# Kernel tuning notes

Hardware: AMD Instinct MI355X
Metric: run time of the kernel (lower is better)

## Reference

```python
import jax, jax.numpy as jnp
import numpy as np

B = 4096          # number of graphs
NPG = 148         # nodes per graph (fixed by ReadOut(num_nodes=148))
N = B * NPG       # total nodes = 606208
EPG = 592         # edges per graph (~avg degree 4: RNA backbone + base pairs)
E = B * EPG       # total edges = 2424832


def setup_inputs() -> dict:
    key = jax.random.key(0)
    ks = jax.random.split(key, 10)
    x = jax.random.normal(ks[0], (N, 4), jnp.float32)
    # edges confined within each graph via per-graph node offsets
    src = jax.random.randint(ks[1], (E,), 0, NPG, dtype=jnp.int32)
    dst = jax.random.randint(ks[2], (E,), 0, NPG, dtype=jnp.int32)
    offs = jnp.repeat(jnp.arange(B, dtype=jnp.int32) * NPG, EPG)
    edge_index = jnp.stack([src + offs, dst + offs], axis=0)
    batch = jnp.repeat(jnp.arange(B, dtype=jnp.int32), NPG)
    # GCNConv weights (glorot-ish) and biases: 4->16->32->64
    def glorot(k, fi, fo):
        return jax.random.normal(k, (fi, fo), jnp.float32) * np.sqrt(2.0 / (fi + fo)).astype(np.float32)
    W1 = glorot(ks[3], 4, 16); b1 = jnp.zeros((16,), jnp.float32)
    W2 = glorot(ks[4], 16, 32); b2 = jnp.zeros((32,), jnp.float32)
    W3 = glorot(ks[5], 32, 64); b3 = jnp.zeros((64,), jnp.float32)
    return {"x": x, "edge_index": edge_index, "batch": batch,
            "W1": W1, "b1": b1, "W2": W2, "b2": b2, "W3": W3, "b3": b3}


def gcn_conv(x, src, dst, W, b, n):
    """PyG GCNConv: x' = D^{-1/2}(A+I)D^{-1/2} (x W) + b."""
    h = x @ W                                   # [n, out]
    loop = jnp.arange(n, dtype=src.dtype)       # self loops
    s = jnp.concatenate([src, loop])
    d = jnp.concatenate([dst, loop])
    deg = jax.ops.segment_sum(jnp.ones_like(s, h.dtype), d, num_segments=n)
    dis = jnp.where(deg > 0, jax.lax.rsqrt(jnp.maximum(deg, 1e-12)), 0.0)
    norm = dis[s] * dis[d]                      # [n_edges_with_loops]
    msg = h[s] * norm[:, None]                  # gather + normalize
    return jax.ops.segment_sum(msg, d, num_segments=n) + b


def reference(x, edge_index, batch, W1, b1, W2, b2, W3, b3):
    src, dst = edge_index[0], edge_index[1]
    n = x.shape[0]
    # Dropout(p=0.1) is identity at inference time
    h = jax.nn.relu(gcn_conv(x, src, dst, W1, b1, n))
    h = jax.nn.relu(gcn_conv(h, src, dst, W2, b2, n))
    h = jax.nn.relu(gcn_conv(h, src, dst, W3, b3, n))
    # to_dense_batch with max_num_nodes=148: every graph has exactly 148 nodes
    # and `batch` is sorted block-constant, so dense batching == reshape.
    dense = h.reshape(B, NPG, h.shape[-1])      # [B, 148, 64]
    return dense.reshape(B, -1)                 # Flatten -> [B, 9472]
```

## Files before the change

### kernel.cpp

```cpp
#include <hip/hip_runtime.h>

#define NPG 148
#define EPG 592
#define NTHR 256
#define SA   40
#define MT   10

typedef _Float16 h8 __attribute__((ext_vector_type(8)));
typedef _Float16 h4 __attribute__((ext_vector_type(4)));
typedef float    f4 __attribute__((ext_vector_type(4)));


template<int Fi, int Fo, int KC, int NTN, int MAXJ, int NSLOT, int WROW, int BOFF, bool LAST>
__device__ __forceinline__ void layer(int t,
    _Float16* __restrict__ A16, const _Float16* __restrict__ Wt,
    const float* __restrict__ s_b, const int* __restrict__ s_csr,
    const int* __restrict__ s_row, const float* __restrict__ s_dis,
    float* __restrict__ gout)
{
    constexpr int GITEMS = NPG * KC;

    float r[NSLOT][8];
    #pragma unroll
    for (int sl = 0; sl < NSLOT; ++sl) {
        const int item = t + sl * NTHR;
        if (item < GITEMS) {
            const int d  = item / KC;
            const int kc = item % KC;
            const h8 hv = *reinterpret_cast<const h8*>(&A16[d * SA + kc * 8]);
            const float dd = s_dis[d];
            float a[8];
            #pragma unroll
            for (int u = 0; u < 8; ++u) a[u] = dd * (float)hv[u];
            const int e1 = s_row[d + 1];
            for (int e = s_row[d]; e < e1; ++e) {
                const int sidx = s_csr[e];
                const float ds = s_dis[sidx];
                const h8 m = *reinterpret_cast<const h8*>(&A16[sidx * SA + kc * 8]);
                #pragma unroll
                for (int u = 0; u < 8; ++u) a[u] = fmaf((float)m[u], ds, a[u]);
            }
            #pragma unroll
            for (int u = 0; u < 8; ++u) r[sl][u] = a[u] * dd;
        }
    }
    __syncthreads();
    #pragma unroll
    for (int sl = 0; sl < NSLOT; ++sl) {
        const int item = t + sl * NTHR;
        if (item < GITEMS) {
            const int d  = item / KC;
            const int kc = item % KC;
            h8 pv;
            #pragma unroll
            for (int u = 0; u < 8; ++u) pv[u] = (_Float16)r[sl][u];
            *reinterpret_cast<h8*>(&A16[d * SA + kc * 8]) = pv;
        }
    }
    __syncthreads();

    const int w   = t >> 6;
    const int l16 = t & 15;
    const int q   = (t >> 4) & 3;
    h8 af[MAXJ], bf[MAXJ];
    #pragma unroll
    for (int j = 0; j < MAXJ; ++j) {
        const int idx = w + 4 * j;
        if (idx < MT * NTN) {
            const int mt = idx / NTN, nt = idx % NTN;
            af[j] = *reinterpret_cast<const h8*>(&A16[(mt * 16 + l16) * SA + q * 8]);
            bf[j] = *reinterpret_cast<const h8*>(&Wt[(WROW + nt * 16 + l16) * SA + q * 8]);
        }
    }
    __syncthreads();
    #pragma unroll
    for (int j = 0; j < MAXJ; ++j) {
        const int idx = w + 4 * j;
        if (idx < MT * NTN) {
            const int mt = idx / NTN, nt = idx % NTN;
            f4 acc = {0.f, 0.f, 0.f, 0.f};
            acc = __builtin_amdgcn_mfma_f32_16x16x32_f16(af[j], bf[j], acc, 0, 0, 0);
            const int col  = nt * 16 + l16;
            const float bias = s_b[BOFF + col];
            #pragma unroll
            for (int rr = 0; rr < 4; ++rr) {
                const float v = fmaxf(acc[rr] + bias, 0.f);
                const int row = mt * 16 + q * 4 + rr;
                if (LAST) {
                    if (row < NPG) gout[row * 64 + col] = v;
                } else {
                    A16[row * SA + col] = (_Float16)v;
                }
            }
        }
    }
    if (!LAST) __syncthreads();
}

__global__ __launch_bounds__(256, 4)
void gcn_fused(const float* __restrict__ x,
               const int* __restrict__ esrc, const int* __restrict__ edst,
               const float* __restrict__ W1, const float* __restrict__ b1,
               const float* __restrict__ W2, const float* __restrict__ b2,
               const float* __restrict__ W3, const float* __restrict__ b3,
               float* __restrict__ out)
{
    __shared__ __align__(16) _Float16 A16[160 * SA];
    __shared__ __align__(16) _Float16 Wt[112 * SA];
    __shared__ float s_b[112];
    __shared__ int   s_csr[EPG];
    __shared__ int   s_edge[EPG];
    __shared__ int   s_row[NPG + 2];
    __shared__ float s_dis[NPG];
    __shared__ int   s_cnt[NPG], s_cnt2[NPG];

    const int t  = threadIdx.x;
    const int g  = blockIdx.x;
    const int be = g * EPG;
    const int bn = g * NPG;

    for (int i = t; i < 160 * SA / 8; i += NTHR) reinterpret_cast<f4*>(A16)[i] = f4{0.f, 0.f, 0.f, 0.f};
    for (int i = t; i < 112 * SA / 8; i += NTHR) reinterpret_cast<f4*>(Wt)[i]  = f4{0.f, 0.f, 0.f, 0.f};
    if (t < NPG) { s_cnt[t] = 0; s_cnt2[t] = 0; }
    __syncthreads();

    for (int e = t; e < EPG; e += NTHR) {
        const int s = esrc[be + e] - bn;
        const int d = edst[be + e] - bn;
        s_edge[e] = s | (d << 8);
        atomicAdd(&s_cnt[d], 1);
    }
    for (int i = t; i < 64;   i += NTHR) Wt[(i & 15) * SA + (i >> 4)]        = (_Float16)W1[i];
    for (int i = t; i < 512;  i += NTHR) Wt[(16 + (i & 31)) * SA + (i >> 5)] = (_Float16)W2[i];
    for (int i = t; i < 2048; i += NTHR) Wt[(48 + (i & 63)) * SA + (i >> 6)] = (_Float16)W3[i];
    if (t < 16)       s_b[t] = b1[t];
    else if (t < 48)  s_b[t] = b2[t - 16];
    else if (t < 112) s_b[t] = b3[t - 48];
    if (t < NPG) {
        const float4 xv = reinterpret_cast<const float4*>(x)[bn + t];
        h4 p; p[0] = (_Float16)xv.x; p[1] = (_Float16)xv.y; p[2] = (_Float16)xv.z; p[3] = (_Float16)xv.w;
        *reinterpret_cast<h4*>(&A16[t * SA]) = p;
    }
    __syncthreads();

    if (t < NPG) s_dis[t] = rsqrtf((float)(s_cnt[t] + 1));
    if (t < 64) {
        const int lane = t;
        int v0 = s_cnt[lane];
        int v1 = s_cnt[64 + lane];
        int v2 = (128 + lane < NPG) ? s_cnt[128 + lane] : 0;
        #pragma unroll
        for (int off = 1; off < 64; off <<= 1) {
            const int u0 = __shfl_up(v0, off);
            const int u1 = __shfl_up(v1, off);
            const int u2 = __shfl_up(v2, off);
            if (lane >= off) { v0 += u0; v1 += u1; v2 += u2; }
        }
        const int t0 = __shfl(v0, 63);
        const int t1 = __shfl(v1, 63);
        v1 += t0;
        v2 += t0 + t1;
        if (lane == 0) s_row[0] = 0;
        s_row[1 + lane]  = v0;
        s_row[65 + lane] = v1;
        if (128 + lane < NPG) s_row[129 + lane] = v2;
    }
    __syncthreads();

    for (int e = t; e < EPG; e += NTHR) {
        const int pk = s_edge[e];
        const int s  = pk & 0xFF;
        const int d  = pk >> 8;
        const int pos = s_row[d] + atomicAdd(&s_cnt2[d], 1);
        s_csr[pos] = s;
    }
    __syncthreads();

    float* gout = out + (size_t)bn * 64;
    layer< 4, 16,  1,  1,   3,   1,    0,   0, false>(t, A16, Wt, s_b, s_csr, s_row, s_dis, gout);
    layer<16, 32,  2,  2,   5,   2,   16,  16, false>(t, A16, Wt, s_b, s_csr, s_row, s_dis, gout);
    layer<32, 64,  4,  4,  10,   3,   48,  48, true >(t, A16, Wt, s_b, s_csr, s_row, s_dis, gout);
}

extern "C" void kernel_launch(void* const* d_in, const int* in_sizes, int n_in,
                              void* d_out, int out_size, void* d_ws, size_t ws_size,
                              hipStream_t stream)
{
    const float* x  = (const float*)d_in[0];
    const int*   ei = (const int*)d_in[1];
    const float* W1 = (const float*)d_in[3];
    const float* b1 = (const float*)d_in[4];
    const float* W2 = (const float*)d_in[5];
    const float* b2 = (const float*)d_in[6];
    const float* W3 = (const float*)d_in[7];
    const float* b3 = (const float*)d_in[8];
    float* out = (float*)d_out;

    const int N = in_sizes[0] / 4;
    const int B = N / NPG;
    const int E = in_sizes[1] / 2;

    gcn_fused<<<B, NTHR, 0, stream>>>(x, ei, ei + E, W1, b1, W2, b2, W3, b3, out);
}
```

Baseline: 66.30 us.

## Pack CSR entries with fp16 norm and sort nodes by degree for balance

Each CSR entry now packs the source node's byte offset together with its fp16 inverse-sqrt degree, so the gather loop needs one shared load per edge instead of two. Nodes are bucket-sorted by in-degree through a small histogram and prefix scan, so threads in a wavefront get similar loop trip counts and diverge less. Per-node metadata (offset, norm, edge range) is packed into a uint2. The launch-bounds occupancy hint is raised from 4 to 5 blocks per CU. In exchange the degree normalisation is stored in fp16 rather than fp32, and the setup phase gains an extra barrier and the sort work.

```diff
diff --git a/kernel.cpp b/kernel.cpp
--- a/kernel.cpp
+++ b/kernel.cpp
@@ -14,29 +14,33 @@
 template<int Fi, int Fo, int KC, int NTN, int MAXJ, int NSLOT, int WROW, int BOFF, bool LAST>
 __device__ __forceinline__ void layer(int t,
     _Float16* __restrict__ A16, const _Float16* __restrict__ Wt,
-    const float* __restrict__ s_b, const int* __restrict__ s_csr,
-    const int* __restrict__ s_row, const float* __restrict__ s_dis,
-    float* __restrict__ gout)
+    const float* __restrict__ s_b, const uint2* __restrict__ s_meta,
+    const unsigned int* __restrict__ s_csr, float* __restrict__ gout)
 {
     constexpr int GITEMS = NPG * KC;
 
     float r[NSLOT][8];
+    int   ro[NSLOT];
     #pragma unroll
     for (int sl = 0; sl < NSLOT; ++sl) {
         const int item = t + sl * NTHR;
         if (item < GITEMS) {
             const int d  = item / KC;
-            const int kc = item % KC;
-            const h8 hv = *reinterpret_cast<const h8*>(&A16[d * SA + kc * 8]);
-            const float dd = s_dis[d];
+            const int kc = item & (KC - 1);
+            const uint2 me = s_meta[d];
+            const int off = (int)(me.x & 0xffffu) + kc * 16;
+            ro[sl] = off;
+            const h8 hv = *reinterpret_cast<const h8*>(reinterpret_cast<const char*>(A16) + off);
+            const float dd = (float)__builtin_bit_cast(_Float16, (unsigned short)(me.x >> 16));
             float a[8];
             #pragma unroll
             for (int u = 0; u < 8; ++u) a[u] = dd * (float)hv[u];
-            const int e1 = s_row[d + 1];
-            for (int e = s_row[d]; e < e1; ++e) {
-                const int sidx = s_csr[e];
-                const float ds = s_dis[sidx];
-                const h8 m = *reinterpret_cast<const h8*>(&A16[sidx * SA + kc * 8]);
+            const int e1 = (int)(me.y >> 16);
+            for (int e = (int)(me.y & 0xffffu); e < e1; ++e) {
+                const unsigned int pk = s_csr[e];
+                const h8 m = *reinterpret_cast<const h8*>(
+                    reinterpret_cast<const char*>(A16) + (pk & 0xffffu) + kc * 16);
+                const float ds = (float)__builtin_bit_cast(_Float16, (unsigned short)(pk >> 16));
                 #pragma unroll
                 for (int u = 0; u < 8; ++u) a[u] = fmaf((float)m[u], ds, a[u]);
             }
@@ -49,12 +53,10 @@
     for (int sl = 0; sl < NSLOT; ++sl) {
         const int item = t + sl * NTHR;
         if (item < GITEMS) {
-            const int d  = item / KC;
-            const int kc = item % KC;
             h8 pv;
             #pragma unroll
             for (int u = 0; u < 8; ++u) pv[u] = (_Float16)r[sl][u];
-            *reinterpret_cast<h8*>(&A16[d * SA + kc * 8]) = pv;
+            *reinterpret_cast<h8*>(reinterpret_cast<char*>(A16) + ro[sl]) = pv;
         }
     }
     __syncthreads();
@@ -97,7 +99,7 @@
     if (!LAST) __syncthreads();
 }
 
-__global__ __launch_bounds__(256, 4)
+__global__ __launch_bounds__(256, 5)
 void gcn_fused(const float* __restrict__ x,
                const int* __restrict__ esrc, const int* __restrict__ edst,
                const float* __restrict__ W1, const float* __restrict__ b1,
@@ -108,11 +110,13 @@
     __shared__ __align__(16) _Float16 A16[160 * SA];
     __shared__ __align__(16) _Float16 Wt[112 * SA];
     __shared__ float s_b[112];
-    __shared__ int   s_csr[EPG];
+    __shared__ unsigned int s_csr[EPG];
     __shared__ int   s_edge[EPG];
     __shared__ int   s_row[NPG + 2];
-    __shared__ float s_dis[NPG];
+    __shared__ unsigned int s_dish[NPG];
+    __shared__ uint2 s_meta[NPG];
     __shared__ int   s_cnt[NPG], s_cnt2[NPG];
+    __shared__ int   s_hist[64], s_boff[64], s_bcnt[64];
 
     const int t  = threadIdx.x;
     const int g  = blockIdx.x;
@@ -122,6 +126,7 @@
     for (int i = t; i < 160 * SA / 8; i += NTHR) reinterpret_cast<f4*>(A16)[i] = f4{0.f, 0.f, 0.f, 0.f};
     for (int i = t; i < 112 * SA / 8; i += NTHR) reinterpret_cast<f4*>(Wt)[i]  = f4{0.f, 0.f, 0.f, 0.f};
     if (t < NPG) { s_cnt[t] = 0; s_cnt2[t] = 0; }
+    if (t < 64)  { s_hist[t] = 0; s_bcnt[t] = 0; }
     __syncthreads();
 
     for (int e = t; e < EPG; e += NTHR) {
@@ -143,7 +148,14 @@
     }
     __syncthreads();
 
-    if (t < NPG) s_dis[t] = rsqrtf((float)(s_cnt[t] + 1));
+    if (t < NPG) {
+        const int deg = s_cnt[t];
+        const float disf = rsqrtf((float)(deg + 1));
+        s_dish[t] = ((unsigned int)__builtin_bit_cast(unsigned short, (_Float16)disf)) << 16;
+        atomicAdd(&s_hist[min(deg, 63)], 1);
+    }
+    __syncthreads();
+
     if (t < 64) {
         const int lane = t;
         int v0 = s_cnt[lane];
@@ -164,6 +176,16 @@
         s_row[1 + lane]  = v0;
         s_row[65 + lane] = v1;
         if (128 + lane < NPG) s_row[129 + lane] = v2;
+    } else if (t < 128) {
+        const int lane = t - 64;
+        const int orig = s_hist[lane];
+        int v = orig;
+        #pragma unroll
+        for (int off = 1; off < 64; off <<= 1) {
+            const int u = __shfl_up(v, off);
+            if (lane >= off) v += u;
+        }
+        s_boff[lane] = v - orig;
     }
     __syncthreads();
 
@@ -172,14 +194,21 @@
         const int s  = pk & 0xFF;
         const int d  = pk >> 8;
         const int pos = s_row[d] + atomicAdd(&s_cnt2[d], 1);
-        s_csr[pos] = s;
+        s_csr[pos] = (unsigned int)(s * (SA * 2)) | s_dish[s];
+    }
+    if (t < NPG) {
+        const int deg = s_cnt[t];
+        const int b   = min(deg, 63);
+        const int p   = s_boff[b] + atomicAdd(&s_bcnt[b], 1);
+        s_meta[p] = make_uint2((unsigned int)(t * (SA * 2)) | s_dish[t],
+                               (unsigned int)s_row[t] | ((unsigned int)s_row[t + 1] << 16));
     }
     __syncthreads();
 
     float* gout = out + (size_t)bn * 64;
-    layer< 4, 16,  1,  1,   3,   1,    0,   0, false>(t, A16, Wt, s_b, s_csr, s_row, s_dis, gout);
-    layer<16, 32,  2,  2,   5,   2,   16,  16, false>(t, A16, Wt, s_b, s_csr, s_row, s_dis, gout);
-    layer<32, 64,  4,  4,  10,   3,   48,  48, true >(t, A16, Wt, s_b, s_csr, s_row, s_dis, gout);
+    layer< 4, 16,  1,  1,   3,   1,    0,   0, false>(t, A16, Wt, s_b, s_meta, s_csr, gout);
+    layer<16, 32,  2,  2,   5,   2,   16,  16, false>(t, A16, Wt, s_b, s_meta, s_csr, gout);
+    layer<32, 64,  4,  4,  10,   3,   48,  48, true >(t, A16, Wt, s_b, s_meta, s_csr, gout);
 }
 
 extern "C" void kernel_launch(void* const* d_in, const int* in_sizes, int n_in,
```

Measured after the change: 63.23 us. 1.05x faster.

## Shrink shared memory, pack CSR entries, and aggregate one node per thread

Applied to the files above, without the earlier changes.

Aliases the edge staging buffer onto the weight tile, stores degree norms, row offsets and biases as 16-bit values, and packs byte offset plus source norm into each CSR entry. This lowers LDS per block so occupancy can rise (launch bounds raised to 6). Aggregation now uses one thread per node covering all feature chunks, with a prefetch of the next CSR entry, instead of one thread per (node, chunk) item. The trade-off is that only 148 of 256 threads work during aggregation, and the fp16 norms and biases lose some precision.

```diff
diff --git a/kernel.cpp b/kernel.cpp
--- a/kernel.cpp
+++ b/kernel.cpp
@@ -10,51 +10,58 @@
 typedef _Float16 h4 __attribute__((ext_vector_type(4)));
 typedef float    f4 __attribute__((ext_vector_type(4)));
 
-
-template<int Fi, int Fo, int KC, int NTN, int MAXJ, int NSLOT, int WROW, int BOFF, bool LAST>
+__device__ __forceinline__ float f16bits_to_f32(unsigned short u) {
+    return (float)__builtin_bit_cast(_Float16, u);
+}
+
+
+template<int Fi, int Fo, int KC, int NTN, int MAXJ, int WROW, int BOFF, bool LAST>
 __device__ __forceinline__ void layer(int t,
     _Float16* __restrict__ A16, const _Float16* __restrict__ Wt,
-    const float* __restrict__ s_b, const int* __restrict__ s_csr,
-    const int* __restrict__ s_row, const float* __restrict__ s_dis,
+    const _Float16* __restrict__ s_bh, const unsigned int* __restrict__ s_csr,
+    const unsigned short* __restrict__ s_row, const unsigned short* __restrict__ s_dis,
     float* __restrict__ gout)
 {
-    constexpr int GITEMS = NPG * KC;
-
-    float r[NSLOT][8];
-    #pragma unroll
-    for (int sl = 0; sl < NSLOT; ++sl) {
-        const int item = t + sl * NTHR;
-        if (item < GITEMS) {
-            const int d  = item / KC;
-            const int kc = item % KC;
-            const h8 hv = *reinterpret_cast<const h8*>(&A16[d * SA + kc * 8]);
-            const float dd = s_dis[d];
-            float a[8];
-            #pragma unroll
-            for (int u = 0; u < 8; ++u) a[u] = dd * (float)hv[u];
-            const int e1 = s_row[d + 1];
-            for (int e = s_row[d]; e < e1; ++e) {
-                const int sidx = s_csr[e];
-                const float ds = s_dis[sidx];
-                const h8 m = *reinterpret_cast<const h8*>(&A16[sidx * SA + kc * 8]);
+    float a[KC][8];
+    if (t < NPG) {
+        const float dd = f16bits_to_f32(s_dis[t]);
+        const char* selfb = reinterpret_cast<const char*>(A16) + t * (SA * 2);
+        #pragma unroll
+        for (int kc = 0; kc < KC; ++kc) {
+            const h8 hv = *reinterpret_cast<const h8*>(selfb + kc * 16);
+            #pragma unroll
+            for (int u = 0; u < 8; ++u) a[kc][u] = dd * (float)hv[u];
+        }
+        int e  = s_row[t];
+        const int e1 = s_row[t + 1];
+        unsigned int pk = (e < e1) ? s_csr[e] : 0u;
+        while (e < e1) {
+            const unsigned int pknext = (e + 1 < e1) ? s_csr[e + 1] : 0u;
+            const char* mb = reinterpret_cast<const char*>(A16) + (pk & 0xffffu);
+            const float ds = f16bits_to_f32((unsigned short)(pk >> 16));
+            #pragma unroll
+            for (int kc = 0; kc < KC; ++kc) {
+                const h8 m = *reinterpret_cast<const h8*>(mb + kc * 16);
                 #pragma unroll
-                for (int u = 0; u < 8; ++u) a[u] = fmaf((float)m[u], ds, a[u]);
+                for (int u = 0; u < 8; ++u) a[kc][u] = fmaf((float)m[u], ds, a[kc][u]);
             }
-            #pragma unroll
-            for (int u = 0; u < 8; ++u) r[sl][u] = a[u] * dd;
-        }
-    }
-    __syncthreads();
-    #pragma unroll
-    for (int sl = 0; sl < NSLOT; ++sl) {
-        const int item = t + sl * NTHR;
-        if (item < GITEMS) {
-            const int d  = item / KC;
-            const int kc = item % KC;
+            pk = pknext;
+            ++e;
+        }
+        #pragma unroll
+        for (int kc = 0; kc < KC; ++kc)
+            #pragma unroll
+            for (int u = 0; u < 8; ++u) a[kc][u] *= dd;
+    }
+    __syncthreads();
+    if (t < NPG) {
+        char* selfb = reinterpret_cast<char*>(A16) + t * (SA * 2);
+        #pragma unroll
+        for (int kc = 0; kc < KC; ++kc) {
             h8 pv;
             #pragma unroll
-            for (int u = 0; u < 8; ++u) pv[u] = (_Float16)r[sl][u];
-            *reinterpret_cast<h8*>(&A16[d * SA + kc * 8]) = pv;
+            for (int u = 0; u < 8; ++u) pv[u] = (_Float16)a[kc][u];
+            *reinterpret_cast<h8*>(selfb + kc * 16) = pv;
         }
     }
     __syncthreads();
@@ -81,7 +88,7 @@
             f4 acc = {0.f, 0.f, 0.f, 0.f};
             acc = __builtin_amdgcn_mfma_f32_16x16x32_f16(af[j], bf[j], acc, 0, 0, 0);
             const int col  = nt * 16 + l16;
-            const float bias = s_b[BOFF + col];
+            const float bias = (float)s_bh[BOFF + col];
             #pragma unroll
             for (int rr = 0; rr < 4; ++rr) {
                 const float v = fmaxf(acc[rr] + bias, 0.f);
@@ -97,7 +104,7 @@
     if (!LAST) __syncthreads();
 }
 
-__global__ __launch_bounds__(256, 4)
+__global__ __launch_bounds__(256, 6)
 void gcn_fused(const float* __restrict__ x,
                const int* __restrict__ esrc, const int* __restrict__ edst,
                const float* __restrict__ W1, const float* __restrict__ b1,
@@ -107,43 +114,35 @@
 {
     __shared__ __align__(16) _Float16 A16[160 * SA];
     __shared__ __align__(16) _Float16 Wt[112 * SA];
-    __shared__ float s_b[112];
-    __shared__ int   s_csr[EPG];
-    __shared__ int   s_edge[EPG];
-    __shared__ int   s_row[NPG + 2];
-    __shared__ float s_dis[NPG];
-    __shared__ int   s_cnt[NPG], s_cnt2[NPG];
+    __shared__ _Float16 s_bh[112];
+    __shared__ unsigned int s_csr[EPG];
+    __shared__ unsigned short s_row[152];
+    __shared__ unsigned short s_dis[NPG];
+    __shared__ int s_cnt[NPG], s_cnt2[NPG];
+
+    int* s_edge = reinterpret_cast<int*>(Wt);
 
     const int t  = threadIdx.x;
     const int g  = blockIdx.x;
     const int be = g * EPG;
     const int bn = g * NPG;
 
-    for (int i = t; i < 160 * SA / 8; i += NTHR) reinterpret_cast<f4*>(A16)[i] = f4{0.f, 0.f, 0.f, 0.f};
-    for (int i = t; i < 112 * SA / 8; i += NTHR) reinterpret_cast<f4*>(Wt)[i]  = f4{0.f, 0.f, 0.f, 0.f};
     if (t < NPG) { s_cnt[t] = 0; s_cnt2[t] = 0; }
-    __syncthreads();
-
     for (int e = t; e < EPG; e += NTHR) {
         const int s = esrc[be + e] - bn;
         const int d = edst[be + e] - bn;
         s_edge[e] = s | (d << 8);
-        atomicAdd(&s_cnt[d], 1);
-    }
-    for (int i = t; i < 64;   i += NTHR) Wt[(i & 15) * SA + (i >> 4)]        = (_Float16)W1[i];
-    for (int i = t; i < 512;  i += NTHR) Wt[(16 + (i & 31)) * SA + (i >> 5)] = (_Float16)W2[i];
-    for (int i = t; i < 2048; i += NTHR) Wt[(48 + (i & 63)) * SA + (i >> 6)] = (_Float16)W3[i];
-    if (t < 16)       s_b[t] = b1[t];
-    else if (t < 48)  s_b[t] = b2[t - 16];
-    else if (t < 112) s_b[t] = b3[t - 48];
-    if (t < NPG) {
-        const float4 xv = reinterpret_cast<const float4*>(x)[bn + t];
-        h4 p; p[0] = (_Float16)xv.x; p[1] = (_Float16)xv.y; p[2] = (_Float16)xv.z; p[3] = (_Float16)xv.w;
-        *reinterpret_cast<h4*>(&A16[t * SA]) = p;
-    }
-    __syncthreads();
-
-    if (t < NPG) s_dis[t] = rsqrtf((float)(s_cnt[t] + 1));
+    }
+    __syncthreads();
+
+    for (int e = t; e < EPG; e += NTHR)
+        atomicAdd(&s_cnt[((unsigned)s_edge[e]) >> 8], 1);
+    __syncthreads();
+
+    if (t < NPG) {
+        const float disf = rsqrtf((float)(s_cnt[t] + 1));
+        s_dis[t] = __builtin_bit_cast(unsigned short, (_Float16)disf);
+    }
     if (t < 64) {
         const int lane = t;
         int v0 = s_cnt[lane];
@@ -161,25 +160,41 @@
         v1 += t0;
         v2 += t0 + t1;
         if (lane == 0) s_row[0] = 0;
-        s_row[1 + lane]  = v0;
-        s_row[65 + lane] = v1;
-        if (128 + lane < NPG) s_row[129 + lane] = v2;
+        s_row[1 + lane]  = (unsigned short)v0;
+        s_row[65 + lane] = (unsigned short)v1;
+        if (128 + lane < NPG) s_row[129 + lane] = (unsigned short)v2;
     }
     __syncthreads();
 
     for (int e = t; e < EPG; e += NTHR) {
         const int pk = s_edge[e];
         const int s  = pk & 0xFF;
-        const int d  = pk >> 8;
-        const int pos = s_row[d] + atomicAdd(&s_cnt2[d], 1);
-        s_csr[pos] = s;
+        const int d  = (unsigned)pk >> 8;
+        const int pos = (int)s_row[d] + atomicAdd(&s_cnt2[d], 1);
+        s_csr[pos] = (unsigned int)(s * (SA * 2)) | ((unsigned int)s_dis[s] << 16);
+    }
+    __syncthreads();
+
+    for (int i = t; i < 160 * SA / 8; i += NTHR) reinterpret_cast<f4*>(A16)[i] = f4{0.f, 0.f, 0.f, 0.f};
+    for (int i = t; i < 112 * SA / 8; i += NTHR) reinterpret_cast<f4*>(Wt)[i]  = f4{0.f, 0.f, 0.f, 0.f};
+    __syncthreads();
+    for (int i = t; i < 64;   i += NTHR) Wt[(i & 15) * SA + (i >> 4)]        = (_Float16)W1[i];
+    for (int i = t; i < 512;  i += NTHR) Wt[(16 + (i & 31)) * SA + (i >> 5)] = (_Float16)W2[i];
+    for (int i = t; i < 2048; i += NTHR) Wt[(48 + (i & 63)) * SA + (i >> 6)] = (_Float16)W3[i];
+    if (t < 16)       s_bh[t] = (_Float16)b1[t];
+    else if (t < 48)  s_bh[t] = (_Float16)b2[t - 16];
+    else if (t < 112) s_bh[t] = (_Float16)b3[t - 48];
+    if (t < NPG) {
+        const float4 xv = reinterpret_cast<const float4*>(x)[bn + t];
+        h4 p; p[0] = (_Float16)xv.x; p[1] = (_Float16)xv.y; p[2] = (_Float16)xv.z; p[3] = (_Float16)xv.w;
+        *reinterpret_cast<h4*>(&A16[t * SA]) = p;
     }
     __syncthreads();
 
     float* gout = out + (size_t)bn * 64;
-    layer< 4, 16,  1,  1,   3,   1,    0,   0, false>(t, A16, Wt, s_b, s_csr, s_row, s_dis, gout);
-    layer<16, 32,  2,  2,   5,   2,   16,  16, false>(t, A16, Wt, s_b, s_csr, s_row, s_dis, gout);
-    layer<32, 64,  4,  4,  10,   3,   48,  48, true >(t, A16, Wt, s_b, s_csr, s_row, s_dis, gout);
+    layer< 4, 16,  1,  1,   3,    0,   0, false>(t, A16, Wt, s_bh, s_csr, s_row, s_dis, gout);
+    layer<16, 32,  2,  2,   5,   16,  16, false>(t, A16, Wt, s_bh, s_csr, s_row, s_dis, gout);
+    layer<32, 64,  4,  4,  10,   48,  48, true >(t, A16, Wt, s_bh, s_csr, s_row, s_dis, gout);
 }
 
 extern "C" void kernel_launch(void* const* d_in, const int* in_sizes, int n_in,
```

Result: faster. 64.96 us (-2.0%).
